# Performance work log

Measured on AMD Instinct MI355X. Metric: run time of the kernel, lower is better.

## Reference

```python
import jax, jax.numpy as jnp
import numpy as np

N_NODES = 100000
N_EDGES = 1600000
IN_DIM = 64
OUT_DIM = 64


def setup_inputs() -> dict:
    key = jax.random.key(0)
    k1, k2, k3, k4, k5, k6 = jax.random.split(key, 6)
    x = jax.random.normal(k1, (N_NODES, IN_DIM), dtype=jnp.float32)
    edge_index = jax.random.randint(k2, (2, N_EDGES), 0, N_NODES, dtype=jnp.int64)
    s = 1.0 / np.sqrt(IN_DIM)
    W = jax.random.uniform(k3, (IN_DIM, OUT_DIM), minval=-s, maxval=s, dtype=jnp.float32)
    b = jax.random.uniform(k4, (OUT_DIM,), minval=-s, maxval=s, dtype=jnp.float32)
    W_lin = jax.random.uniform(k5, (IN_DIM, OUT_DIM), minval=-s, maxval=s, dtype=jnp.float32)
    b_lin = jax.random.uniform(k6, (OUT_DIM,), minval=-s, maxval=s, dtype=jnp.float32)
    return {"x": x, "edge_index": edge_index, "W": W, "b": b, "W_lin": W_lin, "b_lin": b_lin}


def _gcn_conv(x, edge_index, W, b):
    # GCNConv with self-loops and symmetric normalization:
    # out = D^{-1/2} (A + I) D^{-1/2} (x @ W) + b
    n = x.shape[0]
    loop = jnp.arange(n, dtype=edge_index.dtype)
    src = jnp.concatenate([edge_index[0], loop])  # [E+N]
    dst = jnp.concatenate([edge_index[1], loop])  # [E+N]
    deg = jax.ops.segment_sum(jnp.ones_like(src, dtype=x.dtype), dst, num_segments=n)
    dinv = jax.lax.rsqrt(jnp.maximum(deg, 1.0))  # deg >= 1 due to self-loops
    norm = dinv[src] * dinv[dst]                  # [E+N]
    h = x @ W                                     # [N, out]
    msg = h[src] * norm[:, None]                  # gather + scale
    out = jax.ops.segment_sum(msg, dst, num_segments=n)  # scatter-add
    return out + b


def reference(x, edge_index, W, b, W_lin, b_lin):
    # NaOp.forward with with_linear=True: conv(x, edge_index) + linear(x)
    return _gcn_conv(x, edge_index, W, b) + (x @ W_lin + b_lin)
```

## Files before the change

### kernel.cpp

```cpp
#include <hip/hip_runtime.h>

#define NN 100000
#define NE 1600000
#define DIM 64
#define K 782
#define ABLK 6250
#define NTILE 256
#define GCAP 2600

typedef __attribute__((ext_vector_type(8))) short bf16x8;
typedef __attribute__((ext_vector_type(8))) _Float16 f16x8;
typedef __attribute__((ext_vector_type(2))) float f32x2;
typedef __attribute__((ext_vector_type(4))) float f32x4;

__device__ __forceinline__ unsigned short f2bf(float f) {
    union { float f; unsigned u; } c; c.f = f;
    unsigned r = (c.u + 0x7FFFu + ((c.u >> 16) & 1u)) >> 16;
    return (unsigned short)r;
}
__device__ __forceinline__ unsigned short f2h(float f) {
    union { _Float16 h; unsigned short u; } c; c.h = (_Float16)f;
    return c.u;
}
__device__ __forceinline__ void acc8(uint2 v, float& a0, float& a1, float& a2, float& a3,
                                     float& a4, float& a5, float& a6, float& a7) {
    f32x2 d0 = __builtin_amdgcn_cvt_pk_f32_fp8(v.x, false);
    f32x2 d1 = __builtin_amdgcn_cvt_pk_f32_fp8(v.x, true);
    f32x2 d2 = __builtin_amdgcn_cvt_pk_f32_fp8(v.y, false);
    f32x2 d3 = __builtin_amdgcn_cvt_pk_f32_fp8(v.y, true);
    a0 += d0.x; a1 += d0.y; a2 += d1.x; a3 += d1.y;
    a4 += d2.x; a5 += d2.y; a6 += d3.x; a7 += d3.y;
}


__global__ void k_init(int* __restrict__ gcur) {
    int i = blockIdx.x * blockDim.x + threadIdx.x;
    if (i < K) gcur[i] = 0;
}


__global__ __launch_bounds__(1024) void k_binA(const int* __restrict__ ei,
                                               int* __restrict__ gcur,
                                               unsigned* __restrict__ ebuf) {
    __shared__ int hist[1024];
    __shared__ int wsum[16];
    __shared__ int hoff[K];
    __shared__ int gbase[K];
    __shared__ int lcur[K];
    __shared__ unsigned sbufE[ABLK];
    __shared__ unsigned short sbufB[ABLK];

    const int tid = threadIdx.x;
    const int e0 = blockIdx.x * ABLK;

    hist[tid] = 0;
    __syncthreads();

    int pk_[7]; int b_[7]; int myN = 0;
#pragma unroll
    for (int i = 0; i < 7; ++i) {
        int j = i * 1024 + tid;
        if (j < ABLK) {
            int e = e0 + j;
            int dst = ei[NE + e];
            int src = ei[e];
            int b = dst >> 7;
            pk_[myN]  = ((dst & 127) << 17) | src;
            b_[myN]   = b;
            ++myN;
            atomicAdd(&hist[b], 1);
        }
    }
    __syncthreads();

    const int lane = tid & 63;
    const int wid  = tid >> 6;
    int cntv = hist[tid];
    int v = cntv;
#pragma unroll
    for (int off = 1; off < 64; off <<= 1) {
        int t = __shfl_up(v, off);
        if (lane >= off) v += t;
    }
    if (lane == 63) wsum[wid] = v;
    __syncthreads();
    int woff = 0;
#pragma unroll
    for (int u = 0; u < 15; ++u) {
        if (u < wid) woff += wsum[u];
    }
    if (tid < K) {
        int incl = v + woff;
        int ho = incl - cntv;
        hoff[tid] = ho;
        lcur[tid] = ho;
        int claimed = (cntv > 0) ? atomicAdd(&gcur[tid], cntv) : 0;
        gbase[tid] = tid * GCAP + claimed;
    }
    __syncthreads();

    for (int j = 0; j < myN; ++j) {
        int pos = atomicAdd(&lcur[b_[j]], 1);
        sbufE[pos] = (unsigned)pk_[j];
        sbufB[pos] = (unsigned short)b_[j];
    }
    __syncthreads();

    for (int j = tid; j < ABLK; j += 1024) {
        unsigned en = sbufE[j];
        int b = sbufB[j];
        ebuf[gbase[b] + (j - hoff[b])] = en;
    }
}


__global__ __launch_bounds__(512) void k_gemm(
    const float* __restrict__ x, const float* __restrict__ W,
    const float* __restrict__ b, const float* __restrict__ Wl,
    const float* __restrict__ bl, const int* __restrict__ gcur,
    const unsigned* __restrict__ ebuf, int* __restrict__ ldeg,
    unsigned char* __restrict__ g8, unsigned short* __restrict__ linbuf) {
    __shared__ unsigned short WcT[128][72];
    __shared__ int lcnt[128];

    const int tid = threadIdx.x;
    {
        const float4* W4  = (const float4*)W;
        const float4* Wl4 = (const float4*)Wl;
        for (int i = tid; i < 1024; i += 512) {
            int k  = i >> 4;
            int c0 = (i & 15) << 2;
            float4 wv = W4[i];
            float4 lv = Wl4[i];
            WcT[c0 + 0][k] = f2bf(wv.x); WcT[c0 + 1][k] = f2bf(wv.y);
            WcT[c0 + 2][k] = f2bf(wv.z); WcT[c0 + 3][k] = f2bf(wv.w);
            WcT[64 + c0 + 0][k] = f2bf(lv.x); WcT[64 + c0 + 1][k] = f2bf(lv.y);
            WcT[64 + c0 + 2][k] = f2bf(lv.z); WcT[64 + c0 + 3][k] = f2bf(lv.w);
        }
    }
    if (tid < 128) lcnt[tid] = 0;
    __syncthreads();

    const int base = blockIdx.x * GCAP;
    const int mB = gcur[blockIdx.x];
    for (int i = tid; i < mB; i += 512) {
        atomicAdd(&lcnt[ebuf[base + i] >> 17], 1);
    }

    const int wv_  = tid >> 6;
    const int lane = tid & 63;
    const int lr   = lane & 15;
    const int lkb  = (lane >> 4) << 3;

    const int lo   = blockIdx.x << 7;
    const int row0 = lo + wv_ * 16;

    int arow = row0 + lr;
    int arc  = arow < NN ? arow : NN - 1;
    const float* xp = x + (size_t)arc * DIM + lkb;
    float4 p0 = *(const float4*)(xp);
    float4 p1 = *(const float4*)(xp + 4);
    float4 p2 = *(const float4*)(xp + 32);
    float4 p3 = *(const float4*)(xp + 36);
    bf16x8 a0 = {(short)f2bf(p0.x), (short)f2bf(p0.y), (short)f2bf(p0.z), (short)f2bf(p0.w),
                 (short)f2bf(p1.x), (short)f2bf(p1.y), (short)f2bf(p1.z), (short)f2bf(p1.w)};
    bf16x8 a1 = {(short)f2bf(p2.x), (short)f2bf(p2.y), (short)f2bf(p2.z), (short)f2bf(p2.w),
                 (short)f2bf(p3.x), (short)f2bf(p3.y), (short)f2bf(p3.z), (short)f2bf(p3.w)};

    f32x4 acc[8];
#pragma unroll
    for (int ct = 0; ct < 8; ++ct) acc[ct] = (f32x4){0.f, 0.f, 0.f, 0.f};

#pragma unroll
    for (int ct = 0; ct < 8; ++ct) {
        bf16x8 b0 = *(const bf16x8*)&WcT[ct * 16 + lr][lkb];
        bf16x8 b1 = *(const bf16x8*)&WcT[ct * 16 + lr][32 + lkb];
        acc[ct] = __builtin_amdgcn_mfma_f32_16x16x32_bf16(a0, b0, acc[ct], 0, 0, 0);
        acc[ct] = __builtin_amdgcn_mfma_f32_16x16x32_bf16(a1, b1, acc[ct], 0, 0, 0);
    }
    __syncthreads();

    if (wv_ == 0) {
        int c0 = lcnt[lane];
        int c1 = lcnt[64 + lane];
        int v0 = c0;
        for (int off = 1; off < 64; off <<= 1) {
            int t = __shfl_up(v0, off);
            if (lane >= off) v0 += t;
        }
        int tot0 = __shfl(v0, 63);
        int v1 = c1;
        for (int off = 1; off < 64; off <<= 1) {
            int t = __shfl_up(v1, off);
            if (lane >= off) v1 += t;
        }
        int* lp = ldeg + blockIdx.x * 128;
        lp[lane] = v0 - c0;
        lp[64 + lane] = tot0 + v1 - c1;
    }

    float bcv[4];
#pragma unroll
    for (int ct = 0; ct < 4; ++ct) {
        int oc = ct * 16 + lr;
        bcv[ct] = b[oc] + bl[oc];
    }
    const int rbase = row0 + ((lane >> 4) << 2);
#pragma unroll
    for (int i = 0; i < 4; ++i) {
        int r = rbase + i;
        if (r >= NN) continue;
        float dv = rsqrtf((float)(lcnt[r - lo] + 1));
        float gv0 = acc[0][i] * dv, gv1 = acc[1][i] * dv;
        float gv2 = acc[2][i] * dv, gv3 = acc[3][i] * dv;
        unsigned w32 = __builtin_amdgcn_cvt_pk_fp8_f32(gv0, gv1, 0, false);
        w32 = (unsigned)__builtin_amdgcn_cvt_pk_fp8_f32(gv2, gv3, w32, true);
        *(unsigned*)(g8 + ((size_t)r << 6) + (lr << 2)) = w32;
        ushort4 lh;
        lh.x = f2h(acc[4][i] + bcv[0] + dv * gv0);
        lh.y = f2h(acc[5][i] + bcv[1] + dv * gv1);
        lh.z = f2h(acc[6][i] + bcv[2] + dv * gv2);
        lh.w = f2h(acc[7][i] + bcv[3] + dv * gv3);
        *(ushort4*)(linbuf + ((size_t)r << 6) + (lr << 2)) = lh;
    }
}


__global__ __launch_bounds__(1024, 8) void k_gatherB(
    const int* __restrict__ gcur, const unsigned* __restrict__ ebuf,
    const int* __restrict__ ldeg, const unsigned short* __restrict__ linbuf,
    const unsigned char* __restrict__ g8, float* __restrict__ out) {
    __shared__ int lptr[128];
    __shared__ int lcur[128];
    __shared__ unsigned lsrc[GCAP];

    const int tid = threadIdx.x;
    const int lo = blockIdx.x << 7;
    const int base = blockIdx.x * GCAP;
    const int mB = gcur[blockIdx.x];

    if (tid < 128) {
        int v = ldeg[blockIdx.x * 128 + tid];
        lptr[tid] = v;
        lcur[tid] = v;
    }
    __syncthreads();

    for (int i = tid; i < mB; i += 1024) {
        unsigned en = ebuf[base + i];
        int ld = en >> 17;
        int pos = atomicAdd(&lcur[ld], 1);
        lsrc[pos] = en & 0x1FFFFu;
    }
    __syncthreads();

    const int node = tid >> 3;
    const int sub  = tid & 7;
    const int sh   = sub << 3;

    const int gnode = lo + node;
    const int start = lptr[node];
    const int m = lcur[node] - start;

    float a0 = 0.f, a1 = 0.f, a2 = 0.f, a3 = 0.f;
    float a4 = 0.f, a5 = 0.f, a6 = 0.f, a7 = 0.f;

    int t = 0;
    for (; t + 4 <= m; t += 4) {
        int s0 = lsrc[start + t + 0];
        int s1 = lsrc[start + t + 1];
        int s2 = lsrc[start + t + 2];
        int s3 = lsrc[start + t + 3];
        uint2 v0 = *(const uint2*)(g8 + (((size_t)s0) << 6) + sh);
        uint2 v1 = *(const uint2*)(g8 + (((size_t)s1) << 6) + sh);
        uint2 v2 = *(const uint2*)(g8 + (((size_t)s2) << 6) + sh);
        uint2 v3 = *(const uint2*)(g8 + (((size_t)s3) << 6) + sh);
        acc8(v0, a0, a1, a2, a3, a4, a5, a6, a7);
        acc8(v1, a0, a1, a2, a3, a4, a5, a6, a7);
        acc8(v2, a0, a1, a2, a3, a4, a5, a6, a7);
        acc8(v3, a0, a1, a2, a3, a4, a5, a6, a7);
    }
    for (; t < m; ++t) {
        uint2 v = *(const uint2*)(g8 + (((size_t)lsrc[start + t]) << 6) + sh);
        acc8(v, a0, a1, a2, a3, a4, a5, a6, a7);
    }

    if (gnode < NN) {
        float dv = rsqrtf((float)(m + 1));
        f16x8 lf = *(const f16x8*)(linbuf + ((size_t)gnode << 6) + sh);
        float* op = out + ((size_t)gnode << 6) + (sub << 1);
        float2 o0 = {(float)lf[0] + dv * a0, (float)lf[4] + dv * a4};
        float2 o1 = {(float)lf[1] + dv * a1, (float)lf[5] + dv * a5};
        float2 o2 = {(float)lf[2] + dv * a2, (float)lf[6] + dv * a6};
        float2 o3 = {(float)lf[3] + dv * a3, (float)lf[7] + dv * a7};
        *(float2*)(op + 0)  = o0;
        *(float2*)(op + 16) = o1;
        *(float2*)(op + 32) = o2;
        *(float2*)(op + 48) = o3;
    }
}


extern "C" void kernel_launch(void* const* d_in, const int* in_sizes, int n_in,
                              void* d_out, int out_size, void* d_ws, size_t ws_size,
                              hipStream_t stream) {
    const float* x  = (const float*)d_in[0];
    const int*   ei = (const int*)d_in[1];
    const float* W  = (const float*)d_in[2];
    const float* b  = (const float*)d_in[3];
    const float* Wl = (const float*)d_in[4];
    const float* bl = (const float*)d_in[5];
    float* out = (float*)d_out;

    char* ws = (char*)d_ws;
    int*      gcur = (int*)(ws + 0);
    int*      ldeg = (int*)(ws + 4096);
    unsigned* ebuf = (unsigned*)(ws + 1048576);
    unsigned char*  g8     = (unsigned char*)(ws + 10485760);
    unsigned short* linbuf = (unsigned short*)(ws + 17039360);

    k_init   <<<1, 1024, 0, stream>>>(gcur);
    k_binA   <<<NTILE, 1024, 0, stream>>>(ei, gcur, ebuf);
    k_gemm   <<<K, 512, 0, stream>>>(x, W, b, Wl, bl, gcur, ebuf, ldeg, g8, linbuf);
    k_gatherB<<<K, 1024, 0, stream>>>(gcur, ebuf, ldeg, linbuf, g8, out);
}
```

Measured before the change: 66.32 us.

## Build per-block CSR in gemm kernel and drop LDS sort from gather

The gemm kernel now holds its block's edge entries in registers while it counts local degrees, computes offsets, and scatters the source indices back into ebuf in CSR order. It also writes an end pointer using a wider stride. The gather kernel reads start/end offsets and source indices straight from global memory, with no shared-memory counting sort and no barriers. This moves the sort work onto the gemm kernel and adds scattered global writes there, in exchange for a lighter, higher-occupancy gather kernel.

```diff
diff --git a/kernel.cpp b/kernel.cpp
--- a/kernel.cpp
+++ b/kernel.cpp
@@ -7,6 +7,7 @@
 #define ABLK 6250
 #define NTILE 256
 #define GCAP 2600
+#define LSTR 132
 
 typedef __attribute__((ext_vector_type(8))) short bf16x8;
 typedef __attribute__((ext_vector_type(8))) _Float16 f16x8;
@@ -118,10 +119,12 @@
     const float* __restrict__ x, const float* __restrict__ W,
     const float* __restrict__ b, const float* __restrict__ Wl,
     const float* __restrict__ bl, const int* __restrict__ gcur,
-    const unsigned* __restrict__ ebuf, int* __restrict__ ldeg,
+    unsigned* __restrict__ ebuf, int* __restrict__ ldeg,
     unsigned char* __restrict__ g8, unsigned short* __restrict__ linbuf) {
     __shared__ unsigned short WcT[128][72];
     __shared__ int lcnt[128];
+    __shared__ int lptrS[128];
+    __shared__ int lcurS[128];
 
     const int tid = threadIdx.x;
     {
@@ -143,8 +146,17 @@
 
     const int base = blockIdx.x * GCAP;
     const int mB = gcur[blockIdx.x];
-    for (int i = tid; i < mB; i += 512) {
-        atomicAdd(&lcnt[ebuf[base + i] >> 17], 1);
+    unsigned en_[6];
+#pragma unroll
+    for (int i = 0; i < 6; ++i) {
+        int idx = i * 512 + tid;
+        if (idx < mB) {
+            unsigned en = ebuf[base + idx];
+            en_[i] = en;
+            atomicAdd(&lcnt[en >> 17], 1);
+        } else {
+            en_[i] = 0xFFFFFFFFu;
+        }
     }
 
     const int wv_  = tid >> 6;
@@ -194,9 +206,24 @@
             int t = __shfl_up(v1, off);
             if (lane >= off) v1 += t;
         }
-        int* lp = ldeg + blockIdx.x * 128;
-        lp[lane] = v0 - c0;
-        lp[64 + lane] = tot0 + v1 - c1;
+        int e0x = v0 - c0;
+        int e1x = tot0 + v1 - c1;
+        lptrS[lane] = e0x;      lcurS[lane] = e0x;
+        lptrS[64 + lane] = e1x; lcurS[64 + lane] = e1x;
+        int* lp = ldeg + blockIdx.x * LSTR;
+        lp[lane] = e0x;
+        lp[64 + lane] = e1x;
+        if (lane == 63) lp[128] = tot0 + v1;
+    }
+    __syncthreads();
+
+#pragma unroll
+    for (int i = 0; i < 6; ++i) {
+        if (en_[i] != 0xFFFFFFFFu) {
+            int ld = en_[i] >> 17;
+            int pos = atomicAdd(&lcurS[ld], 1);
+            ebuf[base + pos] = en_[i] & 0x1FFFFu;
+        }
     }
 
     float bcv[4];
@@ -227,50 +254,30 @@
 
 
 __global__ __launch_bounds__(1024, 8) void k_gatherB(
-    const int* __restrict__ gcur, const unsigned* __restrict__ ebuf,
-    const int* __restrict__ ldeg, const unsigned short* __restrict__ linbuf,
+    const int* __restrict__ ldeg, const unsigned* __restrict__ csr,
+    const unsigned short* __restrict__ linbuf,
     const unsigned char* __restrict__ g8, float* __restrict__ out) {
-    __shared__ int lptr[128];
-    __shared__ int lcur[128];
-    __shared__ unsigned lsrc[GCAP];
-
-    const int tid = threadIdx.x;
-    const int lo = blockIdx.x << 7;
-    const int base = blockIdx.x * GCAP;
-    const int mB = gcur[blockIdx.x];
-
-    if (tid < 128) {
-        int v = ldeg[blockIdx.x * 128 + tid];
-        lptr[tid] = v;
-        lcur[tid] = v;
-    }
-    __syncthreads();
-
-    for (int i = tid; i < mB; i += 1024) {
-        unsigned en = ebuf[base + i];
-        int ld = en >> 17;
-        int pos = atomicAdd(&lcur[ld], 1);
-        lsrc[pos] = en & 0x1FFFFu;
-    }
-    __syncthreads();
-
+    const int tid  = threadIdx.x;
     const int node = tid >> 3;
     const int sub  = tid & 7;
     const int sh   = sub << 3;
 
-    const int gnode = lo + node;
-    const int start = lptr[node];
-    const int m = lcur[node] - start;
+    const int* lp = ldeg + blockIdx.x * LSTR;
+    const int start = lp[node];
+    const int end   = lp[node + 1];
+    const int m = end - start;
+    const unsigned* cp = csr + blockIdx.x * GCAP + start;
+    const int gnode = (blockIdx.x << 7) + node;
 
     float a0 = 0.f, a1 = 0.f, a2 = 0.f, a3 = 0.f;
     float a4 = 0.f, a5 = 0.f, a6 = 0.f, a7 = 0.f;
 
     int t = 0;
     for (; t + 4 <= m; t += 4) {
-        int s0 = lsrc[start + t + 0];
-        int s1 = lsrc[start + t + 1];
-        int s2 = lsrc[start + t + 2];
-        int s3 = lsrc[start + t + 3];
+        int s0 = cp[t + 0];
+        int s1 = cp[t + 1];
+        int s2 = cp[t + 2];
+        int s3 = cp[t + 3];
         uint2 v0 = *(const uint2*)(g8 + (((size_t)s0) << 6) + sh);
         uint2 v1 = *(const uint2*)(g8 + (((size_t)s1) << 6) + sh);
         uint2 v2 = *(const uint2*)(g8 + (((size_t)s2) << 6) + sh);
@@ -281,7 +288,7 @@
         acc8(v3, a0, a1, a2, a3, a4, a5, a6, a7);
     }
     for (; t < m; ++t) {
-        uint2 v = *(const uint2*)(g8 + (((size_t)lsrc[start + t]) << 6) + sh);
+        uint2 v = *(const uint2*)(g8 + (((size_t)cp[t]) << 6) + sh);
         acc8(v, a0, a1, a2, a3, a4, a5, a6, a7);
     }
 
@@ -322,5 +329,5 @@
     k_init   <<<1, 1024, 0, stream>>>(gcur);
     k_binA   <<<NTILE, 1024, 0, stream>>>(ei, gcur, ebuf);
     k_gemm   <<<K, 512, 0, stream>>>(x, W, b, Wl, bl, gcur, ebuf, ldeg, g8, linbuf);
-    k_gatherB<<<K, 1024, 0, stream>>>(gcur, ebuf, ldeg, linbuf, g8, out);
-}
+    k_gatherB<<<K, 1024, 0, stream>>>(ldeg, ebuf, linbuf, g8, out);
+}
```

Result: slower. 73.98 us (+11.5%).
